# Performance work log

Hardware: AMD Instinct MI355X
Metric: run time of the kernel (lower is better)

## Reference

```python
import jax, jax.numpy as jnp
import numpy as np

B, U, D = 128, 200, 512

def setup_inputs() -> dict:
    key = jax.random.key(0)
    k1, k2, k3 = jax.random.split(key, 3)
    input_real = jax.random.normal(k1, (B, D, D), dtype=jnp.float32)
    input_imag = jax.random.normal(k2, (B, D, D), dtype=jnp.float32)
    # keras 'uniform' initializer: U(-0.05, 0.05); unit_norm constraint normalizes over axes (1,2)
    kernel = jax.random.uniform(k3, (U, D, 2), dtype=jnp.float32, minval=-0.05, maxval=0.05)
    kernel = kernel / jnp.linalg.norm(kernel.reshape(U, -1), axis=1)[:, None, None]
    return {"input_real": input_real, "input_imag": input_imag, "kernel": kernel}

def reference(input_real, input_imag, kernel):
    # kernel: [U, D, 2] -> real/imag measurement vectors
    kr = kernel[:, :, 0]  # [U, D]
    ki = kernel[:, :, 1]  # [U, D]
    # Original: M_real = kr kr^T - ki ki^T ; M_imag = ki kr^T + kr ki^T (outer products per unit)
    # out[b,n] = trace(R_b @ M_real_n) - trace(I_b @ M_imag_n)
    # trace(A @ (u v^T)) = sum_ij A[i,j] u[j] v[i] -> quadratic form, avoids [B,U,D,D] tiles.
    t_real = (jnp.einsum('bij,nj,ni->bn', input_real, kr, kr)
              - jnp.einsum('bij,nj,ni->bn', input_real, ki, ki))
    t_imag = (jnp.einsum('bij,nj,ni->bn', input_imag, ki, kr)
              + jnp.einsum('bij,nj,ni->bn', input_imag, kr, ki))
    return t_real - t_imag  # [B, U]
```

## Files before the change

kernel.cpp:

```cpp
#include <hip/hip_runtime.h>
#include <hip/hip_bf16.h>
#include <string.h>

#define BB 128
#define UU 200
#define DD 512
#define NP 256
#define NWS 504

typedef __attribute__((ext_vector_type(8))) short short8;
typedef __attribute__((ext_vector_type(4))) float f32x4;

__device__ __forceinline__ unsigned pack_bf16_2(float a, float b) {
    __hip_bfloat162 h = __float22bfloat162_rn(make_float2(a, b));
    unsigned u; memcpy(&u, &h, 4); return u;
}

__device__ __forceinline__ unsigned short f2bf(float x) {
    union { float f; unsigned u; } v; v.f = x;
    unsigned r = v.u + 0x7FFFu + ((v.u >> 16) & 1u);
    return (unsigned short)(r >> 16);
}

__global__ void kb_build_kernel(const float* __restrict__ Kt, unsigned* __restrict__ Kb) {
    int idx = blockIdx.x * 256 + threadIdx.x;
    int n = idx >> 9, j = idx & 511;
    unsigned v = 0u;
    if (n < UU) {
        float2 s = ((const float2*)Kt)[(size_t)n * DD + j];
        v = pack_bf16_2(s.x, s.y);
    }
    Kb[idx] = v;
}

__global__ void zero_out_kernel(float* __restrict__ out) {
    int i = blockIdx.x * 256 + threadIdx.x;
    if (i < BB * UU) out[i] = 0.0f;
}

__global__ void reduce_kernel(const float* __restrict__ ws, float* __restrict__ out) {
    int o = blockIdx.x * 256 + threadIdx.x;
    if (o >= BB * UU) return;
    int p0 = blockIdx.y * 36;
    float s = 0.0f;
#pragma unroll
    for (int p = 0; p < 36; ++p)
        s += ws[(size_t)(p0 + p) * (BB * UU) + o];
    atomicAdd(&out[o], s);
}

__global__ __launch_bounds__(1024, 4) void cm_gemm2_kernel(
    const float* __restrict__ Ar, const float* __restrict__ Ai,
    const float* __restrict__ Kt, const unsigned* __restrict__ Kb,
    float* __restrict__ ws, float* __restrict__ out)
{
    __shared__ short sA[2 * 128 * 128];

    const int tid  = threadIdx.x;
    const int irow = blockIdx.x;
    const int w    = tid >> 6;
    const int lane = tid & 63;
    const int rrow = lane & 15;
    const int quad = lane >> 4;
    const int nn   = w * 16 + rrow;
    const int xr   = rrow & 7;

    float krI = 0.f, kiI = 0.f;
    if (nn < UU) {
        float2 s = ((const float2*)Kt)[(size_t)nn * DD + irow];
        krI = s.x; kiI = s.y;
    }
    const float nkrI = -krI, nkiI = -kiI;

    const int g = tid & 31, r0 = tid >> 5;
    unsigned boff[4];
    int waddr[4];
#pragma unroll
    for (int l = 0; l < 4; ++l) {
        int row = r0 + 32 * l;
        boff[l] = (unsigned)row * (DD * DD) + (unsigned)irow * DD + g * 4;
        waddr[l] = row * 128 + (((g >> 1) ^ (row & 7)) * 8) + (g & 1) * 4;
    }

    f32x4 acc[8];
#pragma unroll
    for (int t = 0; t < 8; ++t) acc[t] = (f32x4)(0.f);

    f32x4 pf[4];
#pragma unroll
    for (int l = 0; l < 4; ++l) pf[l] = *(const f32x4*)(Ar + boff[l]);

    short8 bi_sv[4];

    for (int t = 0; t < 8; ++t) {
        const int ph = t & 1;
        const int j0 = (t >> 1) * 128;
        short* sb = &sA[(t & 1) * (128 * 128)];

#pragma unroll
        for (int l = 0; l < 4; ++l) {
            uint2 u;
            u.x = pack_bf16_2(pf[l][0], pf[l][1]);
            u.y = pack_bf16_2(pf[l][2], pf[l][3]);
            *(uint2*)&sb[waddr[l]] = u;
        }
        __syncthreads();

        if (t < 7) {
            const int tn = t + 1;
            const float* P = (tn & 1) ? Ai : Ar;
            const unsigned jn = (unsigned)((tn >> 1) * 128);
#pragma unroll
            for (int l = 0; l < 4; ++l) pf[l] = *(const f32x4*)(P + boff[l] + jn);
        }

        const unsigned* kbp = Kb + (unsigned)nn * DD + j0 + quad * 8;
        uint4 nx0, nx1;
        if (ph == 0) { nx0 = *(const uint4*)kbp; nx1 = *(const uint4*)(kbp + 4); }

#pragma unroll
        for (int kk = 0; kk < 4; ++kk) {
            short8 bfrag;
            if (ph == 0) {
                uint4 c0 = nx0, c1 = nx1;
                if (kk < 3) {
                    nx0 = *(const uint4*)(kbp + (kk + 1) * 32);
                    nx1 = *(const uint4*)(kbp + (kk + 1) * 32 + 4);
                }
                unsigned dw[8] = {c0.x, c0.y, c0.z, c0.w, c1.x, c1.y, c1.z, c1.w};
                float wr[8], wi[8];
#pragma unroll
                for (int e = 0; e < 8; ++e) {
                    union { unsigned u; float f; } a, b;
                    a.u = dw[e] << 16;
                    b.u = dw[e] & 0xFFFF0000u;
                    wr[e] = krI * a.f + nkiI * b.f;
                    wi[e] = nkrI * b.f + nkiI * a.f;
                }
                union { short8 v; unsigned u[4]; } pr, pi;
#pragma unroll
                for (int e = 0; e < 4; ++e) {
                    pr.u[e] = pack_bf16_2(wr[2 * e], wr[2 * e + 1]);
                    pi.u[e] = pack_bf16_2(wi[2 * e], wi[2 * e + 1]);
                }
                bfrag = pr.v;
                bi_sv[kk] = pi.v;
            } else {
                bfrag = bi_sv[kk];
            }

#pragma unroll
            for (int h = 0; h < 2; ++h) {
                short8 af[4];
#pragma unroll
                for (int q = 0; q < 4; ++q) {
                    int row = (h * 4 + q) * 16 + rrow;
                    int gran = (kk * 4 + quad) ^ xr;
                    af[q] = *(const short8*)&sb[row * 128 + gran * 8];
                }
#pragma unroll
                for (int q = 0; q < 4; ++q)
                    acc[h * 4 + q] = __builtin_amdgcn_mfma_f32_16x16x32_bf16(
                        af[q], bfrag, acc[h * 4 + q], 0, 0, 0);
            }
        }
    }

    if (nn < UU) {
        if (irow < NWS) {
            float* wsp = ws + (size_t)irow * (BB * UU);
#pragma unroll
            for (int ti = 0; ti < 8; ++ti) {
                int m = ti * 16 + quad * 4;
#pragma unroll
                for (int r = 0; r < 4; ++r)
                    wsp[(size_t)(m + r) * UU + nn] = acc[ti][r];
            }
        } else {
#pragma unroll
            for (int ti = 0; ti < 8; ++ti) {
                int m = ti * 16 + quad * 4;
#pragma unroll
                for (int r = 0; r < 4; ++r)
                    atomicAdd(&out[(size_t)(m + r) * UU + nn], acc[ti][r]);
            }
        }
    }
}

#define ASTR 40
#define WSTR 40
__global__ __launch_bounds__(512, 4) void cm_gemm_fb_kernel(
    const float* __restrict__ Ar, const float* __restrict__ Ai,
    const float* __restrict__ Kt, float* __restrict__ dst)
{
    __shared__ short sAr[BB * ASTR];
    __shared__ short sAi[BB * ASTR];
    __shared__ short sWr[NP * WSTR];
    __shared__ short sWi[NP * WSTR];
    const int tid = threadIdx.x, irow = blockIdx.x;
    const int w = tid >> 6, lane = tid & 63;
    const int mw = (w & 1) * 64, nw = (w >> 1) * 64;
    const int rrow = lane & 15, quad = lane >> 4;
    const int nW = tid >> 1, jh = (tid & 1) * 16;
    float krI = 0.f, kiI = 0.f;
    if (nW < UU) { float2 s = ((const float2*)Kt)[(size_t)nW * DD + irow]; krI = s.x; kiI = s.y; }
    const int brow0 = tid >> 3, grp = tid & 7;
    const size_t aoff0 = (size_t)brow0 * DD * DD + (size_t)irow * DD + (size_t)grp * 4;
    const size_t aoff1 = aoff0 + (size_t)64 * DD * DD;
    f32x4 acc[4][4];
#pragma unroll
    for (int a = 0; a < 4; ++a)
#pragma unroll
        for (int b = 0; b < 4; ++b) acc[a][b] = (f32x4)(0.f);
    for (int jw = 0; jw < DD; jw += 32) {
        f32x4 vr0 = *(const f32x4*)(Ar + aoff0 + jw);
        f32x4 vr1 = *(const f32x4*)(Ar + aoff1 + jw);
        f32x4 vi0 = *(const f32x4*)(Ai + aoff0 + jw);
        f32x4 vi1 = *(const f32x4*)(Ai + aoff1 + jw);
        union { unsigned short s[4]; uint2 u; } t0, t1, t2, t3;
#pragma unroll
        for (int q = 0; q < 4; ++q) {
            t0.s[q] = f2bf(vr0[q]); t1.s[q] = f2bf(vr1[q]);
            t2.s[q] = f2bf(vi0[q]); t3.s[q] = f2bf(vi1[q]);
        }
        *(uint2*)&sAr[ brow0       * ASTR + grp * 4] = t0.u;
        *(uint2*)&sAr[(brow0 + 64) * ASTR + grp * 4] = t1.u;
        *(uint2*)&sAi[ brow0       * ASTR + grp * 4] = t2.u;
        *(uint2*)&sAi[(brow0 + 64) * ASTR + grp * 4] = t3.u;
        if (nW < UU) {
            const f32x4* kv = (const f32x4*)(Kt + (size_t)nW * DD * 2 + (size_t)(jw + jh) * 2);
#pragma unroll
            for (int q = 0; q < 8; ++q) {
                f32x4 v = kv[q];
                float wr0 = krI * v[0] - kiI * v[1], wi0 = -(krI * v[1] + kiI * v[0]);
                float wr1 = krI * v[2] - kiI * v[3], wi1 = -(krI * v[3] + kiI * v[2]);
                *(unsigned*)&sWr[nW * WSTR + jh + 2 * q] = (unsigned)f2bf(wr0) | ((unsigned)f2bf(wr1) << 16);
                *(unsigned*)&sWi[nW * WSTR + jh + 2 * q] = (unsigned)f2bf(wi0) | ((unsigned)f2bf(wi1) << 16);
            }
        } else {
#pragma unroll
            for (int q = 0; q < 8; ++q) {
                *(unsigned*)&sWr[nW * WSTR + jh + 2 * q] = 0u;
                *(unsigned*)&sWi[nW * WSTR + jh + 2 * q] = 0u;
            }
        }
        __syncthreads();
#pragma unroll
        for (int ph = 0; ph < 2; ++ph) {
            const short* sA = ph ? sAi : sAr;
            const short* sW = ph ? sWi : sWr;
            short8 af[4], bf[4];
#pragma unroll
            for (int t = 0; t < 4; ++t) {
                af[t] = *(const short8*)&sA[(mw + t * 16 + rrow) * ASTR + quad * 8];
                bf[t] = *(const short8*)&sW[(nw + t * 16 + rrow) * WSTR + quad * 8];
            }
#pragma unroll
            for (int ti = 0; ti < 4; ++ti)
#pragma unroll
                for (int tj = 0; tj < 4; ++tj)
                    acc[ti][tj] = __builtin_amdgcn_mfma_f32_16x16x32_bf16(af[ti], bf[tj], acc[ti][tj], 0, 0, 0);
        }
        __syncthreads();
    }
#pragma unroll
    for (int ti = 0; ti < 4; ++ti) {
        int m = mw + ti * 16 + quad * 4;
#pragma unroll
        for (int tj = 0; tj < 4; ++tj) {
            int n = nw + tj * 16 + rrow;
            if (n < UU)
#pragma unroll
                for (int r = 0; r < 4; ++r)
                    atomicAdd(&dst[(size_t)(m + r) * UU + n], acc[ti][tj][r]);
        }
    }
}

extern "C" void kernel_launch(void* const* d_in, const int* in_sizes, int n_in,
                              void* d_out, int out_size, void* d_ws, size_t ws_size,
                              hipStream_t stream) {
    const float* Ar = (const float*)d_in[0];
    const float* Ai = (const float*)d_in[1];
    const float* Kt = (const float*)d_in[2];
    float* out = (float*)d_out;

    const size_t kb_dwords = (size_t)NP * DD;
    const size_t ws_need = kb_dwords * 4 + (size_t)NWS * BB * UU * 4;

    if (ws_size >= ws_need) {
        unsigned* Kb = (unsigned*)d_ws;
        float* ws = (float*)d_ws + kb_dwords;
        hipLaunchKernelGGL(kb_build_kernel, dim3(512), dim3(256), 0, stream, Kt, Kb);
        hipLaunchKernelGGL(zero_out_kernel, dim3(100), dim3(256), 0, stream, out);
        hipLaunchKernelGGL(cm_gemm2_kernel, dim3(DD), dim3(1024), 0, stream,
                           Ar, Ai, Kt, Kb, ws, out);
        hipLaunchKernelGGL(reduce_kernel, dim3(100, 14), dim3(256), 0, stream, ws, out);
    } else {
        hipLaunchKernelGGL(zero_out_kernel, dim3(100), dim3(256), 0, stream, out);
        hipLaunchKernelGGL(cm_gemm_fb_kernel, dim3(DD), dim3(512), 0, stream, Ar, Ai, Kt, out);
    }
}
```

Before: 306.3 us.

## Retile bilinear GEMM to 2x4 wave grid with blocked Kb layout

Replaces the 1024-thread kernel, where each wave owned 16 units across all 128 batch rows, with a 512-thread kernel in which each wave computes a 64x64 output tile (4x4 MFMA accumulators). This reuses each A fragment across four B fragments. The kernel now streams 64-column chunks alternating real and imaginary parts in a padded, swizzled 80-short-stride LDS layout. Kb is rewritten into a 16x8 blocked layout so per-lane B loads are contiguous. B fragments are recomputed for both the real and imaginary phases instead of caching the imaginary ones, which adds ALU work, and the larger accumulator set raises register pressure.

```diff
diff --git a/kernel.cpp b/kernel.cpp
--- a/kernel.cpp
+++ b/kernel.cpp
@@ -30,7 +30,8 @@
         float2 s = ((const float2*)Kt)[(size_t)n * DD + j];
         v = pack_bf16_2(s.x, s.y);
     }
-    Kb[idx] = v;
+    int nb = n >> 4, nl = n & 15, jb = j >> 3, jl = j & 7;
+    Kb[((nb * 64 + jb) << 7) + (nl << 3) + jl] = v;
 }
 
 __global__ void zero_out_kernel(float* __restrict__ out) {
@@ -49,140 +50,164 @@
     atomicAdd(&out[o], s);
 }
 
-__global__ __launch_bounds__(1024, 4) void cm_gemm2_kernel(
+__global__ __launch_bounds__(512, 4) void cm_gemm3_kernel(
     const float* __restrict__ Ar, const float* __restrict__ Ai,
     const float* __restrict__ Kt, const unsigned* __restrict__ Kb,
     float* __restrict__ ws, float* __restrict__ out)
 {
-    __shared__ short sA[2 * 128 * 128];
+    __shared__ short sA[2][128 * 80];
 
     const int tid  = threadIdx.x;
     const int irow = blockIdx.x;
     const int w    = tid >> 6;
     const int lane = tid & 63;
+    const int wm   = w & 1;
+    const int wn   = w >> 1;
+    const int m0   = wm * 64;
+    const int n0   = wn * 64;
+    const int nb0  = n0 >> 4;
     const int rrow = lane & 15;
     const int quad = lane >> 4;
-    const int nn   = w * 16 + rrow;
-    const int xr   = rrow & 7;
-
-    float krI = 0.f, kiI = 0.f;
-    if (nn < UU) {
-        float2 s = ((const float2*)Kt)[(size_t)nn * DD + irow];
-        krI = s.x; kiI = s.y;
-    }
-    const float nkrI = -krI, nkiI = -kiI;
-
-    const int g = tid & 31, r0 = tid >> 5;
-    unsigned boff[4];
-    int waddr[4];
-#pragma unroll
-    for (int l = 0; l < 4; ++l) {
-        int row = r0 + 32 * l;
-        boff[l] = (unsigned)row * (DD * DD) + (unsigned)irow * DD + g * 4;
-        waddr[l] = row * 128 + (((g >> 1) ^ (row & 7)) * 8) + (g & 1) * 4;
-    }
-
-    f32x4 acc[8];
-#pragma unroll
-    for (int t = 0; t < 8; ++t) acc[t] = (f32x4)(0.f);
+
+    float krI[4], kiI[4];
+#pragma unroll
+    for (int t = 0; t < 4; ++t) {
+        int n = n0 + t * 16 + rrow;
+        if (n < UU) {
+            float2 kv = ((const float2*)Kt)[(size_t)n * DD + irow];
+            krI[t] = kv.x; kiI[t] = kv.y;
+        } else { krI[t] = 0.f; kiI[t] = 0.f; }
+    }
+
+    const int srow = tid >> 2;
+    const int p    = tid & 3;
+    const int hs   = (srow ^ (srow >> 3)) & 7;
+    const size_t abase = (size_t)srow * (DD * DD) + (size_t)irow * DD + p * 16;
+    const int wa0 = srow * 80 + (((2 * p)     ^ hs) * 8);
+    const int wa1 = srow * 80 + (((2 * p + 1) ^ hs) * 8);
+
+    int ra[4][2];
+#pragma unroll
+    for (int t = 0; t < 4; ++t) {
+        int m  = m0 + t * 16 + rrow;
+        int hm = (m ^ (m >> 3)) & 7;
+        ra[t][0] = m * 80 + ((quad       ^ hm) * 8);
+        ra[t][1] = m * 80 + (((4 + quad) ^ hm) * 8);
+    }
+
+    f32x4 acc[4][4];
+#pragma unroll
+    for (int a = 0; a < 4; ++a)
+#pragma unroll
+        for (int b = 0; b < 4; ++b) acc[a][b] = (f32x4)(0.f);
 
     f32x4 pf[4];
 #pragma unroll
-    for (int l = 0; l < 4; ++l) pf[l] = *(const f32x4*)(Ar + boff[l]);
-
-    short8 bi_sv[4];
-
-    for (int t = 0; t < 8; ++t) {
-        const int ph = t & 1;
-        const int j0 = (t >> 1) * 128;
-        short* sb = &sA[(t & 1) * (128 * 128)];
-
-#pragma unroll
-        for (int l = 0; l < 4; ++l) {
-            uint2 u;
-            u.x = pack_bf16_2(pf[l][0], pf[l][1]);
-            u.y = pack_bf16_2(pf[l][2], pf[l][3]);
-            *(uint2*)&sb[waddr[l]] = u;
-        }
-        __syncthreads();
-
-        if (t < 7) {
-            const int tn = t + 1;
-            const float* P = (tn & 1) ? Ai : Ar;
-            const unsigned jn = (unsigned)((tn >> 1) * 128);
-#pragma unroll
-            for (int l = 0; l < 4; ++l) pf[l] = *(const f32x4*)(P + boff[l] + jn);
-        }
-
-        const unsigned* kbp = Kb + (unsigned)nn * DD + j0 + quad * 8;
-        uint4 nx0, nx1;
-        if (ph == 0) { nx0 = *(const uint4*)kbp; nx1 = *(const uint4*)(kbp + 4); }
-
-#pragma unroll
-        for (int kk = 0; kk < 4; ++kk) {
-            short8 bfrag;
+    for (int l = 0; l < 4; ++l) pf[l] = *(const f32x4*)(Ar + abase + l * 4);
+
+    for (int c = 0; c < 8; ++c) {
+#pragma unroll
+        for (int ph = 0; ph < 2; ++ph) {
+            short* sb = sA[ph];
+
+            uint4 g0, g1;
+            g0.x = pack_bf16_2(pf[0][0], pf[0][1]);
+            g0.y = pack_bf16_2(pf[0][2], pf[0][3]);
+            g0.z = pack_bf16_2(pf[1][0], pf[1][1]);
+            g0.w = pack_bf16_2(pf[1][2], pf[1][3]);
+            g1.x = pack_bf16_2(pf[2][0], pf[2][1]);
+            g1.y = pack_bf16_2(pf[2][2], pf[2][3]);
+            g1.z = pack_bf16_2(pf[3][0], pf[3][1]);
+            g1.w = pack_bf16_2(pf[3][2], pf[3][3]);
+            *(uint4*)&sb[wa0] = g0;
+            *(uint4*)&sb[wa1] = g1;
+            __syncthreads();
+
             if (ph == 0) {
-                uint4 c0 = nx0, c1 = nx1;
-                if (kk < 3) {
-                    nx0 = *(const uint4*)(kbp + (kk + 1) * 32);
-                    nx1 = *(const uint4*)(kbp + (kk + 1) * 32 + 4);
+#pragma unroll
+                for (int l = 0; l < 4; ++l)
+                    pf[l] = *(const f32x4*)(Ai + abase + c * 64 + l * 4);
+            } else if (c < 7) {
+#pragma unroll
+                for (int l = 0; l < 4; ++l)
+                    pf[l] = *(const f32x4*)(Ar + abase + (c + 1) * 64 + l * 4);
+            }
+
+            float P[4], Q[4];
+#pragma unroll
+            for (int t = 0; t < 4; ++t) {
+                P[t] = ph ? -kiI[t] : krI[t];
+                Q[t] = ph ? -krI[t] : -kiI[t];
+            }
+
+            const unsigned kbase = (unsigned)(nb0 * 8192) + (unsigned)((c * 8 + quad) * 128) + (unsigned)(rrow * 8);
+            uint4 nxa = *(const uint4*)(Kb + kbase);
+            uint4 nxb = *(const uint4*)(Kb + kbase + 4);
+
+#pragma unroll
+            for (int kk = 0; kk < 2; ++kk) {
+                short8 af[4];
+#pragma unroll
+                for (int t = 0; t < 4; ++t)
+                    af[t] = *(const short8*)&sb[ra[t][kk]];
+
+#pragma unroll
+                for (int tj = 0; tj < 4; ++tj) {
+                    uint4 ca = nxa, cb = nxb;
+                    if (!(kk == 1 && tj == 3)) {
+                        int tn = (tj == 3) ? 0 : tj + 1;
+                        int kn = (tj == 3) ? 1 : kk;
+                        unsigned na = kbase + (unsigned)(tn * 8192) + (unsigned)(kn * 512);
+                        nxa = *(const uint4*)(Kb + na);
+                        nxb = *(const uint4*)(Kb + na + 4);
+                    }
+                    unsigned dw[8] = {ca.x, ca.y, ca.z, ca.w, cb.x, cb.y, cb.z, cb.w};
+                    union { short8 v; unsigned u[4]; } bfr;
+#pragma unroll
+                    for (int e2 = 0; e2 < 4; ++e2) {
+                        union { unsigned u; float f; } a0, b0, a1, b1;
+                        a0.u = dw[2 * e2]     << 16;  b0.u = dw[2 * e2]     & 0xFFFF0000u;
+                        a1.u = dw[2 * e2 + 1] << 16;  b1.u = dw[2 * e2 + 1] & 0xFFFF0000u;
+                        float w0 = P[tj] * a0.f + Q[tj] * b0.f;
+                        float w1 = P[tj] * a1.f + Q[tj] * b1.f;
+                        bfr.u[e2] = pack_bf16_2(w0, w1);
+                    }
+#pragma unroll
+                    for (int ti = 0; ti < 4; ++ti)
+                        acc[ti][tj] = __builtin_amdgcn_mfma_f32_16x16x32_bf16(
+                            af[ti], bfr.v, acc[ti][tj], 0, 0, 0);
                 }
-                unsigned dw[8] = {c0.x, c0.y, c0.z, c0.w, c1.x, c1.y, c1.z, c1.w};
-                float wr[8], wi[8];
-#pragma unroll
-                for (int e = 0; e < 8; ++e) {
-                    union { unsigned u; float f; } a, b;
-                    a.u = dw[e] << 16;
-                    b.u = dw[e] & 0xFFFF0000u;
-                    wr[e] = krI * a.f + nkiI * b.f;
-                    wi[e] = nkrI * b.f + nkiI * a.f;
+            }
+        }
+    }
+
+    if (irow < NWS) {
+        float* wsp = ws + (size_t)irow * (BB * UU);
+#pragma unroll
+        for (int ti = 0; ti < 4; ++ti) {
+            int m = m0 + ti * 16 + quad * 4;
+#pragma unroll
+            for (int tj = 0; tj < 4; ++tj) {
+                int n = n0 + tj * 16 + rrow;
+                if (n < UU) {
+#pragma unroll
+                    for (int r = 0; r < 4; ++r)
+                        wsp[(size_t)(m + r) * UU + n] = acc[ti][tj][r];
                 }
-                union { short8 v; unsigned u[4]; } pr, pi;
-#pragma unroll
-                for (int e = 0; e < 4; ++e) {
-                    pr.u[e] = pack_bf16_2(wr[2 * e], wr[2 * e + 1]);
-                    pi.u[e] = pack_bf16_2(wi[2 * e], wi[2 * e + 1]);
+            }
+        }
+    } else {
+#pragma unroll
+        for (int ti = 0; ti < 4; ++ti) {
+            int m = m0 + ti * 16 + quad * 4;
+#pragma unroll
+            for (int tj = 0; tj < 4; ++tj) {
+                int n = n0 + tj * 16 + rrow;
+                if (n < UU) {
+#pragma unroll
+                    for (int r = 0; r < 4; ++r)
+                        atomicAdd(&out[(size_t)(m + r) * UU + n], acc[ti][tj][r]);
                 }
-                bfrag = pr.v;
-                bi_sv[kk] = pi.v;
-            } else {
-                bfrag = bi_sv[kk];
-            }
-
-#pragma unroll
-            for (int h = 0; h < 2; ++h) {
-                short8 af[4];
-#pragma unroll
-                for (int q = 0; q < 4; ++q) {
-                    int row = (h * 4 + q) * 16 + rrow;
-                    int gran = (kk * 4 + quad) ^ xr;
-                    af[q] = *(const short8*)&sb[row * 128 + gran * 8];
-                }
-#pragma unroll
-                for (int q = 0; q < 4; ++q)
-                    acc[h * 4 + q] = __builtin_amdgcn_mfma_f32_16x16x32_bf16(
-                        af[q], bfrag, acc[h * 4 + q], 0, 0, 0);
-            }
-        }
-    }
-
-    if (nn < UU) {
-        if (irow < NWS) {
-            float* wsp = ws + (size_t)irow * (BB * UU);
-#pragma unroll
-            for (int ti = 0; ti < 8; ++ti) {
-                int m = ti * 16 + quad * 4;
-#pragma unroll
-                for (int r = 0; r < 4; ++r)
-                    wsp[(size_t)(m + r) * UU + nn] = acc[ti][r];
-            }
-        } else {
-#pragma unroll
-            for (int ti = 0; ti < 8; ++ti) {
-                int m = ti * 16 + quad * 4;
-#pragma unroll
-                for (int r = 0; r < 4; ++r)
-                    atomicAdd(&out[(size_t)(m + r) * UU + nn], acc[ti][r]);
             }
         }
     }
@@ -248,13 +273,13 @@
         __syncthreads();
 #pragma unroll
         for (int ph = 0; ph < 2; ++ph) {
-            const short* sA = ph ? sAi : sAr;
-            const short* sW = ph ? sWi : sWr;
+            const short* sAp = ph ? sAi : sAr;
+            const short* sWp = ph ? sWi : sWr;
             short8 af[4], bf[4];
 #pragma unroll
             for (int t = 0; t < 4; ++t) {
-                af[t] = *(const short8*)&sA[(mw + t * 16 + rrow) * ASTR + quad * 8];
-                bf[t] = *(const short8*)&sW[(nw + t * 16 + rrow) * WSTR + quad * 8];
+                af[t] = *(const short8*)&sAp[(mw + t * 16 + rrow) * ASTR + quad * 8];
+                bf[t] = *(const short8*)&sWp[(nw + t * 16 + rrow) * WSTR + quad * 8];
             }
 #pragma unroll
             for (int ti = 0; ti < 4; ++ti)
@@ -294,7 +319,7 @@
         float* ws = (float*)d_ws + kb_dwords;
         hipLaunchKernelGGL(kb_build_kernel, dim3(512), dim3(256), 0, stream, Kt, Kb);
         hipLaunchKernelGGL(zero_out_kernel, dim3(100), dim3(256), 0, stream, out);
-        hipLaunchKernelGGL(cm_gemm2_kernel, dim3(DD), dim3(1024), 0, stream,
+        hipLaunchKernelGGL(cm_gemm3_kernel, dim3(DD), dim3(512), 0, stream,
                            Ar, Ai, Kt, Kb, ws, out);
         hipLaunchKernelGGL(reduce_kernel, dim3(100, 14), dim3(256), 0, stream, ws, out);
     } else {
```

Result: slower. 484.8 us (+58.3%).
